# Kernel tuning notes

Measured on AMD Instinct MI355X. Metric: run time of the kernel, lower is better.

## Reference

```python
import jax, jax.numpy as jnp
import numpy as np

N_NODES = 50000
N_EDGES = 1_600_000
F_IN = 128
HIDDEN = 128
N_REL = 8
N_GRAPHS = 64


def setup_inputs() -> dict:
    key = jax.random.key(0)
    ks = jax.random.split(key, 16)
    x = jax.random.normal(ks[0], (N_NODES, F_IN), dtype=jnp.float32)
    edge_index = jax.random.randint(ks[1], (2, N_EDGES), 0, N_NODES, dtype=jnp.int32)
    edge_type = jax.random.randint(ks[2], (N_EDGES,), 0, N_REL, dtype=jnp.int32)
    edge_attr = jax.nn.one_hot(edge_type, N_REL, dtype=jnp.float32)  # one-hot relation encoding
    batch = jnp.sort(jax.random.randint(ks[3], (N_NODES,), 0, N_GRAPHS, dtype=jnp.int32))
    s = 1.0 / np.sqrt(F_IN)
    params = {}
    dims = [(F_IN, HIDDEN), (HIDDEN, HIDDEN), (HIDDEN, HIDDEN)]
    for i, (fi, fo) in enumerate(dims, 1):
        params[f"W{i}"] = jax.random.normal(ks[3 + 3 * i], (N_REL, fi, fo), dtype=jnp.float32) * s
        params[f"root{i}"] = jax.random.normal(ks[4 + 3 * i], (fi, fo), dtype=jnp.float32) * s
        params[f"b{i}"] = jnp.zeros((fo,), dtype=jnp.float32)
    lin_w = jax.random.normal(ks[13], (HIDDEN, HIDDEN), dtype=jnp.float32) * (1.0 / np.sqrt(HIDDEN))
    lin_b = jnp.zeros((HIDDEN,), dtype=jnp.float32)
    return {"x": x, "edge_index": edge_index, "edge_attr": edge_attr, "batch": batch,
            **params, "lin_w": lin_w, "lin_b": lin_b}


def _rgcn_conv(x, src, dst, edge_type, W, root, bias):
    # PyG RGCNConv with aggr='mean': per-relation mean of transformed neighbors + root + bias.
    # Mean is linear, so aggregate raw features per (dst, relation) then apply W_r.
    n = x.shape[0]
    seg = dst * N_REL + edge_type                      # combined segment id [E]
    msg = x[src]                                       # [E, F_in] gather
    agg = jax.ops.segment_sum(msg, seg, num_segments=n * N_REL)
    cnt = jax.ops.segment_sum(jnp.ones((src.shape[0],), x.dtype), seg, num_segments=n * N_REL)
    agg = agg / jnp.maximum(cnt, 1.0)[:, None]
    agg = agg.reshape(n, N_REL, -1)                    # [N, R, F_in]
    return jnp.einsum('nri,rio->no', agg, W) + x @ root + bias


def reference(x, edge_index, edge_attr, batch,
              W1, root1, b1, W2, root2, b2, W3, root3, b3, lin_w, lin_b):
    src, dst = edge_index[0], edge_index[1]
    edge_type = jnp.argmax(edge_attr, axis=1)          # np.where(edge_attr == 1)[1]
    h = jax.nn.relu(_rgcn_conv(x, src, dst, edge_type, W1, root1, b1))
    h = jax.nn.relu(_rgcn_conv(h, src, dst, edge_type, W2, root2, b2))
    h = jax.nn.relu(_rgcn_conv(h, src, dst, edge_type, W3, root3, b3))
    # global_mean_pool over graphs
    sums = jax.ops.segment_sum(h, batch, num_segments=N_GRAPHS)
    cnts = jax.ops.segment_sum(jnp.ones((h.shape[0],), h.dtype), batch, num_segments=N_GRAPHS)
    pooled = sums / jnp.maximum(cnts, 1.0)[:, None]    # [G, hidden]
    return pooled @ lin_w + lin_b
```

## Files before the change

kernel.cpp:

```cpp
#include <hip/hip_runtime.h>
#include <hip/hip_fp16.h>

#define N_NODESC 50000
#define N_EDGESC 1600000
#define FEAT 128
#define NREL 8
#define NSEG (N_NODESC * NREL)
#define NGRAPH 64
#define KTOT 1152
#define NKC 36
#define WPACK_ELEMS (NKC * 4 * 128 * 8)
#define NHALF (N_NODESC * FEAT)

typedef float f32x4 __attribute__((ext_vector_type(4)));
typedef _Float16 f16x8 __attribute__((ext_vector_type(8)));

static inline size_t align256(size_t x) { return (x + 255) & ~(size_t)255; }

__device__ __forceinline__ float4 h4tof4(uint2 r) {
  const __half* h = (const __half*)&r;
  return make_float4(__half2float(h[0]), __half2float(h[1]),
                     __half2float(h[2]), __half2float(h[3]));
}

__global__ void k_zero(int* __restrict__ p, int n) {
  int i = blockIdx.x * blockDim.x + threadIdx.x;
  int stride = gridDim.x * blockDim.x;
  for (; i < n; i += stride) p[i] = 0;
}

__global__ void k_cvt16(const float* __restrict__ in, __half* __restrict__ o) {
  int i = blockIdx.x * blockDim.x + threadIdx.x;
  if (i * 4 >= NHALF) return;
  float4 v = *(const float4*)&in[i * 4];
  __half h[4] = {__float2half(v.x), __float2half(v.y), __float2half(v.z), __float2half(v.w)};
  *(uint2*)&o[(size_t)i * 4] = *(uint2*)h;
}

__global__ void k_edge_hist(const int* __restrict__ ei, const float* __restrict__ eattr,
                            int* __restrict__ seg, int* __restrict__ cnt) {
  int e = blockIdx.x * blockDim.x + threadIdx.x;
  if (e >= N_EDGESC) return;
  int dst = ei[N_EDGESC + e];
  const float4* ap = (const float4*)(eattr + (size_t)e * 8);
  float4 a0 = ap[0], a1 = ap[1];
  int ty = 0;
  if (a0.y > 0.5f) ty = 1;
  if (a0.z > 0.5f) ty = 2;
  if (a0.w > 0.5f) ty = 3;
  if (a1.x > 0.5f) ty = 4;
  if (a1.y > 0.5f) ty = 5;
  if (a1.z > 0.5f) ty = 6;
  if (a1.w > 0.5f) ty = 7;
  int s = dst * NREL + ty;
  seg[e] = s;
  atomicAdd(&cnt[s], 1);
}

__global__ void k_scan1(const int* __restrict__ cnt, int* __restrict__ outIncl,
                        int* __restrict__ bsums, int n) {
  __shared__ int sd[256];
  int t = threadIdx.x;
  int base = blockIdx.x * 4096 + t * 16;
  int v[16];
  int s = 0;
#pragma unroll
  for (int j = 0; j < 16; ++j) {
    int idx = base + j;
    int x = (idx < n) ? cnt[idx] : 0;
    s += x;
    v[j] = s;
  }
  sd[t] = s;
  __syncthreads();
  for (int off = 1; off < 256; off <<= 1) {
    int add = (t >= off) ? sd[t - off] : 0;
    __syncthreads();
    sd[t] += add;
    __syncthreads();
  }
  int prev = (t > 0) ? sd[t - 1] : 0;
#pragma unroll
  for (int j = 0; j < 16; ++j) {
    int idx = base + j;
    if (idx < n) outIncl[idx] = prev + v[j];
  }
  if (t == 255) bsums[blockIdx.x] = sd[255];
}

__global__ void k_scan2(int* __restrict__ bsums, int nb) {
  __shared__ int sd[128];
  int t = threadIdx.x;
  int v = (t < nb) ? bsums[t] : 0;
  sd[t] = v;
  __syncthreads();
  for (int off = 1; off < 128; off <<= 1) {
    int add = (t >= off) ? sd[t - off] : 0;
    __syncthreads();
    sd[t] += add;
    __syncthreads();
  }
  if (t < nb) bsums[t] = sd[t] - v;
}

__global__ void k_scan3(int* __restrict__ offsets, const int* __restrict__ bsums, int n) {
  int i = blockIdx.x * blockDim.x + threadIdx.x;
  if (i == 0) offsets[0] = 0;
  if (i < n) offsets[i + 1] += bsums[i >> 12];
}

__global__ void k_scatter(const int* __restrict__ ei, const int* __restrict__ seg,
                          const int* __restrict__ offsets, int* __restrict__ cursor,
                          int* __restrict__ ssrc) {
  int e = blockIdx.x * blockDim.x + threadIdx.x;
  if (e >= N_EDGESC) return;
  int s = seg[e];
  int p = offsets[s] + atomicAdd(&cursor[s], 1);
  ssrc[p] = ei[e];
}

__global__ __launch_bounds__(256, 8) void k_agg(
    const __half* __restrict__ in, const int* __restrict__ offsets,
    const int* __restrict__ ssrc, __half* __restrict__ agg,
    int nodeBase, int nodeCount) {
  int t = blockIdx.x * blockDim.x + threadIdx.x;
  int un = t >> 5;
  int l = t & 31;
  if (un >= nodeCount) return;
  int node = nodeBase + un;
  for (int r = 0; r < NREL; ++r) {
    int sidx = node * NREL + r;
    int beg = offsets[sidx], end = offsets[sidx + 1];
    float4 s = make_float4(0.f, 0.f, 0.f, 0.f);
    for (int base = beg; base < end; base += 4) {
      int last = end - 1;
      int e1 = base + 1 <= last ? base + 1 : last;
      int e2 = base + 2 <= last ? base + 2 : last;
      int e3 = base + 3 <= last ? base + 3 : last;
      int i0 = ssrc[base], i1 = ssrc[e1], i2 = ssrc[e2], i3 = ssrc[e3];
      uint2 r0 = *(const uint2*)&in[(size_t)i0 * FEAT + l * 4];
      uint2 r1 = *(const uint2*)&in[(size_t)i1 * FEAT + l * 4];
      uint2 r2 = *(const uint2*)&in[(size_t)i2 * FEAT + l * 4];
      uint2 r3 = *(const uint2*)&in[(size_t)i3 * FEAT + l * 4];
      float4 v0 = h4tof4(r0), v1 = h4tof4(r1), v2 = h4tof4(r2), v3 = h4tof4(r3);
      s.x += v0.x; s.y += v0.y; s.z += v0.z; s.w += v0.w;
      if (base + 1 < end) { s.x += v1.x; s.y += v1.y; s.z += v1.z; s.w += v1.w; }
      if (base + 2 < end) { s.x += v2.x; s.y += v2.y; s.z += v2.z; s.w += v2.w; }
      if (base + 3 < end) { s.x += v3.x; s.y += v3.y; s.z += v3.z; s.w += v3.w; }
    }
    int c = end - beg;
    if (c > 1) {
      float inv = 1.0f / (float)c;
      s.x *= inv; s.y *= inv; s.z *= inv; s.w *= inv;
    }
    __half hv[4] = {__float2half(s.x), __float2half(s.y), __float2half(s.z), __float2half(s.w)};
    *(uint2*)&agg[((size_t)un * NREL + r) * FEAT + l * 4] = *(uint2*)hv;
  }
}

__global__ void k_wpack(const float* __restrict__ W, const float* __restrict__ root,
                        __half* __restrict__ whi, __half* __restrict__ wlo) {
  int idx = blockIdx.x * 256 + threadIdx.x;
  if (idx >= WPACK_ELEMS) return;
  int j = idx & 7;
  int n = (idx >> 3) & 127;
  int slot = idx >> 10;
  int k = slot * 8 + j;
  float v = (k < 1024) ? W[(size_t)k * 128 + n] : root[(size_t)(k - 1024) * 128 + n];
  __half hi = __float2half(v);
  float lof = v - __half2float(hi);
  whi[idx] = hi;
  wlo[idx] = __float2half(lof);
}

__global__ __launch_bounds__(256, 3) void k_gemm_mfma(
    const __half* __restrict__ aggc,
    const __half* __restrict__ xin,
    const __half* __restrict__ Whi, const __half* __restrict__ Wlo,
    const float* __restrict__ bias, __half* __restrict__ out16,
    int n0g, int rows) {
  __shared__ __half Ah[2][4096] __attribute__((aligned(16)));
  __shared__ __half Bh[2][4096] __attribute__((aligned(16)));
  __shared__ __half Bl[2][4096] __attribute__((aligned(16)));

  const int t = threadIdx.x;
  const int lane = t & 63, wave = t >> 6;
  const int l15 = lane & 15, lg = lane >> 4;
  const int wrow0 = wave * 32;
  const int m0 = blockIdx.x * 128;
  const int srow = t >> 1, half = t & 1;

  int rowc = srow;
  if (m0 + rowc >= rows) rowc = rows - 1 - m0;
  if (rowc < 0) rowc = 0;
  const __half* aggRow = aggc + (size_t)(m0 + rowc) * 1024 + half * 16;
  const __half* xRow = xin + (size_t)(n0g + m0 + rowc) * FEAT + half * 16;

  uint4 av0, av1, sbh0, sbh1, sbl0, sbl1;

#define LOADC(kc)                                                         \
  {                                                                       \
    const __half* asrc = ((kc) < 32) ? (aggRow + (kc) * 32)               \
                                     : (xRow + ((kc) - 32) * 32);         \
    av0 = ((const uint4*)asrc)[0];                                        \
    av1 = ((const uint4*)asrc)[1];                                        \
    const uint4* bhs = (const uint4*)(Whi + (size_t)(kc) * 4096);         \
    const uint4* bls = (const uint4*)(Wlo + (size_t)(kc) * 4096);         \
    sbh0 = bhs[t * 2]; sbh1 = bhs[t * 2 + 1];                             \
    sbl0 = bls[t * 2]; sbl1 = bls[t * 2 + 1];                             \
  }
#define WRITEC(b)                                                         \
  {                                                                       \
    int g0 = half * 2;                                                    \
    *(uint4*)&Ah[b][(g0 * 128 + srow) * 8] = av0;                         \
    *(uint4*)&Ah[b][((g0 + 1) * 128 + srow) * 8] = av1;                   \
    ((uint4*)Bh[b])[t * 2] = sbh0; ((uint4*)Bh[b])[t * 2 + 1] = sbh1;     \
    ((uint4*)Bl[b])[t * 2] = sbl0; ((uint4*)Bl[b])[t * 2 + 1] = sbl1;     \
  }

  f32x4 acc[2][8];
#pragma unroll
  for (int a = 0; a < 2; ++a)
#pragma unroll
    for (int b = 0; b < 8; ++b) acc[a][b] = (f32x4){0.f, 0.f, 0.f, 0.f};

  LOADC(0);
  WRITEC(0);
  LOADC(1);
  __syncthreads();

  for (int kc = 0; kc < NKC; ++kc) {
    const int cur = kc & 1;
    f16x8 af[2];
#pragma unroll
    for (int mf = 0; mf < 2; ++mf) {
      int ar = wrow0 + mf * 16 + l15;
      af[mf] = *(const f16x8*)&Ah[cur][(lg * 128 + ar) * 8];
    }
#pragma unroll
    for (int nf = 0; nf < 8; ++nf) {
      int bn = nf * 16 + l15;
      f16x8 vh = *(const f16x8*)&Bh[cur][(lg * 128 + bn) * 8];
      f16x8 vl = *(const f16x8*)&Bl[cur][(lg * 128 + bn) * 8];
      acc[0][nf] = __builtin_amdgcn_mfma_f32_16x16x32_f16(af[0], vh, acc[0][nf], 0, 0, 0);
      acc[0][nf] = __builtin_amdgcn_mfma_f32_16x16x32_f16(af[0], vl, acc[0][nf], 0, 0, 0);
      acc[1][nf] = __builtin_amdgcn_mfma_f32_16x16x32_f16(af[1], vh, acc[1][nf], 0, 0, 0);
      acc[1][nf] = __builtin_amdgcn_mfma_f32_16x16x32_f16(af[1], vl, acc[1][nf], 0, 0, 0);
    }
    if (kc < NKC - 1) {
      WRITEC(cur ^ 1);
      if (kc < NKC - 2) LOADC(kc + 2);
      __syncthreads();
    }
  }
#undef LOADC
#undef WRITEC

  float bcol[8];
#pragma unroll
  for (int nf = 0; nf < 8; ++nf) bcol[nf] = bias[nf * 16 + l15];
#pragma unroll
  for (int mf = 0; mf < 2; ++mf)
#pragma unroll
    for (int nf = 0; nf < 8; ++nf)
#pragma unroll
      for (int j = 0; j < 4; ++j) {
        int grow = m0 + wrow0 + mf * 16 + lg * 4 + j;
        if (grow < rows) {
          float v = acc[mf][nf][j] + bcol[nf];
          v = v > 0.f ? v : 0.f;
          out16[(size_t)(n0g + grow) * FEAT + nf * 16 + l15] = __float2half(v);
        }
      }
}

__global__ void k_pool(const __half* __restrict__ h, const int* __restrict__ batch,
                       const float* __restrict__ lw, const float* __restrict__ lb,
                       float* __restrict__ out) {
  __shared__ float sums[8][128];
  __shared__ float prow[128];
  int gidx = blockIdx.x, t = threadIdx.x;
  int f = t & 127, grp = t >> 7;
  int lo = 0, hi = N_NODESC;
  while (lo < hi) {
    int mid = (lo + hi) >> 1;
    if (batch[mid] < gidx) lo = mid + 1; else hi = mid;
  }
  int start = lo;
  hi = N_NODESC;
  while (lo < hi) {
    int mid = (lo + hi) >> 1;
    if (batch[mid] < gidx + 1) lo = mid + 1; else hi = mid;
  }
  int end = lo;
  float s = 0.f;
  for (int n = start + grp; n < end; n += 8) s += __half2float(h[(size_t)n * FEAT + f]);
  sums[grp][f] = s;
  __syncthreads();
  if (grp == 0) {
    float tot = 0.f;
#pragma unroll
    for (int gg = 0; gg < 8; ++gg) tot += sums[gg][f];
    int c = end - start;
    prow[f] = (c > 0) ? tot / (float)c : 0.f;
  }
  __syncthreads();
  float a = 0.f;
  for (int k = grp * 16; k < grp * 16 + 16; ++k) a = fmaf(prow[k], lw[(size_t)k * FEAT + f], a);
  __syncthreads();
  sums[grp][f] = a;
  __syncthreads();
  if (grp == 0) {
    float tot = lb[f];
#pragma unroll
    for (int gg = 0; gg < 8; ++gg) tot += sums[gg][f];
    out[(size_t)gidx * FEAT + f] = tot;
  }
}

extern "C" void kernel_launch(void* const* d_in, const int* in_sizes, int n_in,
                              void* d_out, int out_size, void* d_ws, size_t ws_size,
                              hipStream_t stream) {
  const float* x = (const float*)d_in[0];
  const int* ei = (const int*)d_in[1];
  const float* eattr = (const float*)d_in[2];
  const int* batch = (const int*)d_in[3];
  const float* Wl[3] = {(const float*)d_in[4], (const float*)d_in[7], (const float*)d_in[10]};
  const float* rl[3] = {(const float*)d_in[5], (const float*)d_in[8], (const float*)d_in[11]};
  const float* bl[3] = {(const float*)d_in[6], (const float*)d_in[9], (const float*)d_in[12]};
  const float* lw = (const float*)d_in[13];
  const float* lb = (const float*)d_in[14];
  float* out = (float*)d_out;
  (void)n_in; (void)in_sizes; (void)out_size;

  size_t pos = 0;
  char* base = (char*)d_ws;
  auto alloc = [&](size_t bytes) { char* q = base + pos; pos += align256(bytes); return q; };
  int* seg = (int*)alloc(sizeof(int) * (size_t)N_EDGESC);
  int* cntcur = (int*)alloc(sizeof(int) * (size_t)2 * NSEG);
  int* cnt = cntcur;
  int* cursor = cntcur + NSEG;
  int* offsets = (int*)alloc(sizeof(int) * (size_t)(NSEG + 1));
  int* bsums = (int*)alloc(sizeof(int) * 1024);
  int* ssrc = (int*)alloc(sizeof(int) * (size_t)N_EDGESC);
  __half* p0 = (__half*)alloc(sizeof(__half) * (size_t)NHALF);
  __half* p1 = (__half*)alloc(sizeof(__half) * (size_t)NHALF);
  __half* whi = (__half*)alloc(sizeof(__half) * (size_t)WPACK_ELEMS);
  __half* wlo = (__half*)alloc(sizeof(__half) * (size_t)WPACK_ELEMS);
  size_t remain = (ws_size > pos) ? (ws_size - pos) : 0;
  long long cn = (long long)(remain / (sizeof(__half) * NREL * FEAT));
  int chunkNodes = (cn > N_NODESC) ? N_NODESC : (int)cn;
  chunkNodes &= ~127;
  if (chunkNodes < 128) chunkNodes = 128;
  __half* aggbuf = (__half*)(base + pos);
  int nchunks = (N_NODESC + chunkNodes - 1) / chunkNodes;

  hipLaunchKernelGGL(k_zero, dim3(2048), dim3(256), 0, stream, cntcur, 2 * NSEG);
  hipLaunchKernelGGL(k_edge_hist, dim3((N_EDGESC + 255) / 256), dim3(256), 0, stream,
                     ei, eattr, seg, cnt);
  int nbScan = (NSEG + 4095) / 4096;
  hipLaunchKernelGGL(k_scan1, dim3(nbScan), dim3(256), 0, stream, cnt, offsets + 1, bsums, NSEG);
  hipLaunchKernelGGL(k_scan2, dim3(1), dim3(128), 0, stream, bsums, nbScan);
  hipLaunchKernelGGL(k_scan3, dim3((NSEG + 255) / 256), dim3(256), 0, stream, offsets, bsums, NSEG);
  hipLaunchKernelGGL(k_scatter, dim3((N_EDGESC + 255) / 256), dim3(256), 0, stream,
                     ei, seg, offsets, cursor, ssrc);

  hipLaunchKernelGGL(k_cvt16, dim3((NHALF / 4 + 255) / 256), dim3(256), 0, stream, x, p0);

  const __half* inPtr = p0;
  __half* outPtr = p1;
  for (int L = 0; L < 3; ++L) {
    hipLaunchKernelGGL(k_wpack, dim3((WPACK_ELEMS + 255) / 256), dim3(256), 0, stream,
                       Wl[L], rl[L], whi, wlo);
    for (int c = 0; c < nchunks; ++c) {
      int nodeBase = c * chunkNodes;
      int rowsC = N_NODESC - nodeBase;
      if (rowsC > chunkNodes) rowsC = chunkNodes;
      int aggBlocks = (rowsC * 32 + 255) / 256;
      hipLaunchKernelGGL(k_agg, dim3(aggBlocks), dim3(256), 0, stream,
                         inPtr, offsets, ssrc, aggbuf, nodeBase, rowsC);
      hipLaunchKernelGGL(k_gemm_mfma, dim3((rowsC + 127) / 128), dim3(256), 0, stream,
                         aggbuf, inPtr, whi, wlo, bl[L], outPtr, nodeBase, rowsC);
    }
    const __half* tmp = inPtr;
    inPtr = outPtr;
    outPtr = (__half*)tmp;
  }

  hipLaunchKernelGGL(k_pool, dim3(NGRAPH), dim3(1024), 0, stream, p1, batch, lw, lb, out);
}
```

Measured before the change: 744.6 us.

## Halve GEMM row tile to 64 and pack all layer weights in one prep kernel

```diff
diff --git a/kernel.cpp b/kernel.cpp
--- a/kernel.cpp
+++ b/kernel.cpp
@@ -10,7 +10,9 @@
 #define KTOT 1152
 #define NKC 36
 #define WPACK_ELEMS (NKC * 4 * 128 * 8)
+#define WPACK_BLKS (WPACK_ELEMS / 256)
 #define NHALF (N_NODESC * FEAT)
+#define CVT_BLKS ((NHALF / 4 + 255) / 256)
 
 typedef float f32x4 __attribute__((ext_vector_type(4)));
 typedef _Float16 f16x8 __attribute__((ext_vector_type(8)));
@@ -27,14 +29,6 @@
   int i = blockIdx.x * blockDim.x + threadIdx.x;
   int stride = gridDim.x * blockDim.x;
   for (; i < n; i += stride) p[i] = 0;
-}
-
-__global__ void k_cvt16(const float* __restrict__ in, __half* __restrict__ o) {
-  int i = blockIdx.x * blockDim.x + threadIdx.x;
-  if (i * 4 >= NHALF) return;
-  float4 v = *(const float4*)&in[i * 4];
-  __half h[4] = {__float2half(v.x), __float2half(v.y), __float2half(v.z), __float2half(v.w)};
-  *(uint2*)&o[(size_t)i * 4] = *(uint2*)h;
 }
 
 __global__ void k_edge_hist(const int* __restrict__ ei, const float* __restrict__ eattr,
@@ -117,6 +111,38 @@
   int s = seg[e];
   int p = offsets[s] + atomicAdd(&cursor[s], 1);
   ssrc[p] = ei[e];
+}
+
+__global__ void k_prep(const float* __restrict__ W1, const float* __restrict__ r1,
+                       const float* __restrict__ W2, const float* __restrict__ r2,
+                       const float* __restrict__ W3, const float* __restrict__ r3,
+                       const float* __restrict__ x,
+                       __half* __restrict__ whi3, __half* __restrict__ wlo3,
+                       __half* __restrict__ p0) {
+  int b = blockIdx.x;
+  if (b < 3 * WPACK_BLKS) {
+    int L = b / WPACK_BLKS;
+    int idx = (b - L * WPACK_BLKS) * 256 + threadIdx.x;
+    const float* W = (L == 0) ? W1 : (L == 1) ? W2 : W3;
+    const float* root = (L == 0) ? r1 : (L == 1) ? r2 : r3;
+    int j = idx & 7;
+    int n = (idx >> 3) & 127;
+    int slot = idx >> 10;
+    int k = slot * 8 + j;
+    float v = (k < 1024) ? W[(size_t)k * 128 + n] : root[(size_t)(k - 1024) * 128 + n];
+    __half hi = __float2half(v);
+    float lof = v - __half2float(hi);
+    whi3[(size_t)L * WPACK_ELEMS + idx] = hi;
+    wlo3[(size_t)L * WPACK_ELEMS + idx] = __float2half(lof);
+  } else {
+    int i = (b - 3 * WPACK_BLKS) * 256 + threadIdx.x;
+    if (i * 4 < NHALF) {
+      float4 v = *(const float4*)&x[i * 4];
+      __half h[4] = {__float2half(v.x), __float2half(v.y),
+                     __float2half(v.z), __float2half(v.w)};
+      *(uint2*)&p0[(size_t)i * 4] = *(uint2*)h;
+    }
+  }
 }
 
 __global__ __launch_bounds__(256, 8) void k_agg(
@@ -158,52 +184,36 @@
   }
 }
 
-__global__ void k_wpack(const float* __restrict__ W, const float* __restrict__ root,
-                        __half* __restrict__ whi, __half* __restrict__ wlo) {
-  int idx = blockIdx.x * 256 + threadIdx.x;
-  if (idx >= WPACK_ELEMS) return;
-  int j = idx & 7;
-  int n = (idx >> 3) & 127;
-  int slot = idx >> 10;
-  int k = slot * 8 + j;
-  float v = (k < 1024) ? W[(size_t)k * 128 + n] : root[(size_t)(k - 1024) * 128 + n];
-  __half hi = __float2half(v);
-  float lof = v - __half2float(hi);
-  whi[idx] = hi;
-  wlo[idx] = __float2half(lof);
-}
-
-__global__ __launch_bounds__(256, 3) void k_gemm_mfma(
+__global__ __launch_bounds__(256, 4) void k_gemm_mfma(
     const __half* __restrict__ aggc,
     const __half* __restrict__ xin,
     const __half* __restrict__ Whi, const __half* __restrict__ Wlo,
     const float* __restrict__ bias, __half* __restrict__ out16,
     int n0g, int rows) {
-  __shared__ __half Ah[2][4096] __attribute__((aligned(16)));
+  __shared__ __half Ah[2][2048] __attribute__((aligned(16)));
   __shared__ __half Bh[2][4096] __attribute__((aligned(16)));
   __shared__ __half Bl[2][4096] __attribute__((aligned(16)));
 
   const int t = threadIdx.x;
   const int lane = t & 63, wave = t >> 6;
   const int l15 = lane & 15, lg = lane >> 4;
-  const int wrow0 = wave * 32;
-  const int m0 = blockIdx.x * 128;
-  const int srow = t >> 1, half = t & 1;
+  const int wrow0 = wave * 16;
+  const int m0 = blockIdx.x * 64;
+  const int srow = t >> 2, sseg = t & 3;
 
   int rowc = srow;
   if (m0 + rowc >= rows) rowc = rows - 1 - m0;
   if (rowc < 0) rowc = 0;
-  const __half* aggRow = aggc + (size_t)(m0 + rowc) * 1024 + half * 16;
-  const __half* xRow = xin + (size_t)(n0g + m0 + rowc) * FEAT + half * 16;
-
-  uint4 av0, av1, sbh0, sbh1, sbl0, sbl1;
+  const __half* aggRow = aggc + (size_t)(m0 + rowc) * 1024 + sseg * 8;
+  const __half* xRow = xin + (size_t)(n0g + m0 + rowc) * FEAT + sseg * 8;
+
+  uint4 av0, sbh0, sbh1, sbl0, sbl1;
 
 #define LOADC(kc)                                                         \
   {                                                                       \
     const __half* asrc = ((kc) < 32) ? (aggRow + (kc) * 32)               \
                                      : (xRow + ((kc) - 32) * 32);         \
-    av0 = ((const uint4*)asrc)[0];                                        \
-    av1 = ((const uint4*)asrc)[1];                                        \
+    av0 = *(const uint4*)asrc;                                            \
     const uint4* bhs = (const uint4*)(Whi + (size_t)(kc) * 4096);         \
     const uint4* bls = (const uint4*)(Wlo + (size_t)(kc) * 4096);         \
     sbh0 = bhs[t * 2]; sbh1 = bhs[t * 2 + 1];                             \
@@ -211,18 +221,14 @@
   }
 #define WRITEC(b)                                                         \
   {                                                                       \
-    int g0 = half * 2;                                                    \
-    *(uint4*)&Ah[b][(g0 * 128 + srow) * 8] = av0;                         \
-    *(uint4*)&Ah[b][((g0 + 1) * 128 + srow) * 8] = av1;                   \
+    *(uint4*)&Ah[b][(sseg * 64 + srow) * 8] = av0;                        \
     ((uint4*)Bh[b])[t * 2] = sbh0; ((uint4*)Bh[b])[t * 2 + 1] = sbh1;     \
     ((uint4*)Bl[b])[t * 2] = sbl0; ((uint4*)Bl[b])[t * 2 + 1] = sbl1;     \
   }
 
-  f32x4 acc[2][8];
-#pragma unroll
-  for (int a = 0; a < 2; ++a)
-#pragma unroll
-    for (int b = 0; b < 8; ++b) acc[a][b] = (f32x4){0.f, 0.f, 0.f, 0.f};
+  f32x4 acc[8];
+#pragma unroll
+  for (int b = 0; b < 8; ++b) acc[b] = (f32x4){0.f, 0.f, 0.f, 0.f};
 
   LOADC(0);
   WRITEC(0);
@@ -231,21 +237,14 @@
 
   for (int kc = 0; kc < NKC; ++kc) {
     const int cur = kc & 1;
-    f16x8 af[2];
-#pragma unroll
-    for (int mf = 0; mf < 2; ++mf) {
-      int ar = wrow0 + mf * 16 + l15;
-      af[mf] = *(const f16x8*)&Ah[cur][(lg * 128 + ar) * 8];
-    }
+    f16x8 af = *(const f16x8*)&Ah[cur][(lg * 64 + wrow0 + l15) * 8];
 #pragma unroll
     for (int nf = 0; nf < 8; ++nf) {
       int bn = nf * 16 + l15;
       f16x8 vh = *(const f16x8*)&Bh[cur][(lg * 128 + bn) * 8];
       f16x8 vl = *(const f16x8*)&Bl[cur][(lg * 128 + bn) * 8];
-      acc[0][nf] = __builtin_amdgcn_mfma_f32_16x16x32_f16(af[0], vh, acc[0][nf], 0, 0, 0);
-      acc[0][nf] = __builtin_amdgcn_mfma_f32_16x16x32_f16(af[0], vl, acc[0][nf], 0, 0, 0);
-      acc[1][nf] = __builtin_amdgcn_mfma_f32_16x16x32_f16(af[1], vh, acc[1][nf], 0, 0, 0);
-      acc[1][nf] = __builtin_amdgcn_mfma_f32_16x16x32_f16(af[1], vl, acc[1][nf], 0, 0, 0);
+      acc[nf] = __builtin_amdgcn_mfma_f32_16x16x32_f16(af, vh, acc[nf], 0, 0, 0);
+      acc[nf] = __builtin_amdgcn_mfma_f32_16x16x32_f16(af, vl, acc[nf], 0, 0, 0);
     }
     if (kc < NKC - 1) {
       WRITEC(cur ^ 1);
@@ -260,18 +259,16 @@
 #pragma unroll
   for (int nf = 0; nf < 8; ++nf) bcol[nf] = bias[nf * 16 + l15];
 #pragma unroll
-  for (int mf = 0; mf < 2; ++mf)
-#pragma unroll
-    for (int nf = 0; nf < 8; ++nf)
-#pragma unroll
-      for (int j = 0; j < 4; ++j) {
-        int grow = m0 + wrow0 + mf * 16 + lg * 4 + j;
-        if (grow < rows) {
-          float v = acc[mf][nf][j] + bcol[nf];
-          v = v > 0.f ? v : 0.f;
-          out16[(size_t)(n0g + grow) * FEAT + nf * 16 + l15] = __float2half(v);
-        }
+  for (int nf = 0; nf < 8; ++nf)
+#pragma unroll
+    for (int j = 0; j < 4; ++j) {
+      int grow = m0 + wrow0 + lg * 4 + j;
+      if (grow < rows) {
+        float v = acc[nf][j] + bcol[nf];
+        v = v > 0.f ? v : 0.f;
+        out16[(size_t)(n0g + grow) * FEAT + nf * 16 + l15] = __float2half(v);
       }
+    }
 }
 
 __global__ void k_pool(const __half* __restrict__ h, const int* __restrict__ batch,
@@ -345,8 +342,8 @@
   int* ssrc = (int*)alloc(sizeof(int) * (size_t)N_EDGESC);
   __half* p0 = (__half*)alloc(sizeof(__half) * (size_t)NHALF);
   __half* p1 = (__half*)alloc(sizeof(__half) * (size_t)NHALF);
-  __half* whi = (__half*)alloc(sizeof(__half) * (size_t)WPACK_ELEMS);
-  __half* wlo = (__half*)alloc(sizeof(__half) * (size_t)WPACK_ELEMS);
+  __half* whi3 = (__half*)alloc(sizeof(__half) * (size_t)3 * WPACK_ELEMS);
+  __half* wlo3 = (__half*)alloc(sizeof(__half) * (size_t)3 * WPACK_ELEMS);
   size_t remain = (ws_size > pos) ? (ws_size - pos) : 0;
   long long cn = (long long)(remain / (sizeof(__half) * NREL * FEAT));
   int chunkNodes = (cn > N_NODESC) ? N_NODESC : (int)cn;
@@ -365,13 +362,14 @@
   hipLaunchKernelGGL(k_scatter, dim3((N_EDGESC + 255) / 256), dim3(256), 0, stream,
                      ei, seg, offsets, cursor, ssrc);
 
-  hipLaunchKernelGGL(k_cvt16, dim3((NHALF / 4 + 255) / 256), dim3(256), 0, stream, x, p0);
+  hipLaunchKernelGGL(k_prep, dim3(3 * WPACK_BLKS + CVT_BLKS), dim3(256), 0, stream,
+                     Wl[0], rl[0], Wl[1], rl[1], Wl[2], rl[2], x, whi3, wlo3, p0);
 
   const __half* inPtr = p0;
   __half* outPtr = p1;
   for (int L = 0; L < 3; ++L) {
-    hipLaunchKernelGGL(k_wpack, dim3((WPACK_ELEMS + 255) / 256), dim3(256), 0, stream,
-                       Wl[L], rl[L], whi, wlo);
+    const __half* whi = whi3 + (size_t)L * WPACK_ELEMS;
+    const __half* wlo = wlo3 + (size_t)L * WPACK_ELEMS;
     for (int c = 0; c < nchunks; ++c) {
       int nodeBase = c * chunkNodes;
       int rowsC = N_NODESC - nodeBase;
@@ -379,7 +377,7 @@
       int aggBlocks = (rowsC * 32 + 255) / 256;
       hipLaunchKernelGGL(k_agg, dim3(aggBlocks), dim3(256), 0, stream,
                          inPtr, offsets, ssrc, aggbuf, nodeBase, rowsC);
-      hipLaunchKernelGGL(k_gemm_mfma, dim3((rowsC + 127) / 128), dim3(256), 0, stream,
+      hipLaunchKernelGGL(k_gemm_mfma, dim3((rowsC + 63) / 64), dim3(256), 0, stream,
                          aggbuf, inPtr, whi, wlo, bl[L], outPtr, nodeBase, rowsC);
     }
     const __half* tmp = inPtr;
```

Measured after the change: 753.7 us. No clear change (+1.2%).
